# Kernel optimization log

Measured on AMD Instinct MI355X. Metric: run time of the kernel, lower is better.

The kernel has to match this reference:

```python
import jax, jax.numpy as jnp
import numpy as np

NBOXES = 4096
MAX_BS = 128
NDIM = 3
NPAIRS = 8192
INV4PI = 0.07957747154594767  # 1/(4*pi), 3D Laplace kernel constant


def setup_inputs() -> dict:
    key = jax.random.key(0)
    k1, k2, k3, k4 = jax.random.split(key, 4)
    q_vec = jax.random.normal(k1, (NBOXES, MAX_BS), dtype=jnp.float32)
    XX_list = jax.random.uniform(k2, (NBOXES, MAX_BS, NDIM), dtype=jnp.float32)
    bs_list = jax.random.randint(k3, (NBOXES,), 0, MAX_BS, dtype=jnp.int32)
    uq_boxes = jax.random.randint(k4, (NPAIRS, 2), 0, NBOXES, dtype=jnp.int32)
    return {"q_vec": q_vec, "XX_list": XX_list, "bs_list": bs_list, "uq_boxes": uq_boxes}


def reference(q_vec, XX_list, bs_list, uq_boxes):
    # Batched gather-kernel-matvec-scatter translation (addto_translation with
    # self_bool=False, kappa=0 => 3D Laplace kernel 1/(4*pi*r)).
    nboxes, max_bs = q_vec.shape
    u_boxes = uq_boxes[:, 0]
    q_boxes = uq_boxes[:, 1]

    Xu = XX_list[u_boxes]  # [P, B, 3] gather target points
    Xq = XX_list[q_boxes]  # [P, B, 3] gather source points

    # pairwise squared distances without materializing [P,B,B,3] diffs
    nu = jnp.sum(Xu * Xu, axis=-1)  # [P, B]
    nq = jnp.sum(Xq * Xq, axis=-1)  # [P, B]
    r2 = nu[:, :, None] + nq[:, None, :] - 2.0 * jnp.einsum('pid,pjd->pij', Xu, Xq)
    r2 = jnp.maximum(r2, 0.0)
    nz = r2 > 0.0
    K = jnp.where(nz, INV4PI / jnp.sqrt(jnp.where(nz, r2, 1.0)), 0.0)  # [P, B, B]

    cols = jnp.arange(max_bs, dtype=jnp.int32)
    col_mask = (cols[None, :] < bs_list[q_boxes][:, None]).astype(q_vec.dtype)  # valid src pts
    row_mask = (cols[None, :] < bs_list[u_boxes][:, None]).astype(q_vec.dtype)  # valid trg pts

    qv = q_vec[q_boxes] * col_mask                         # gather + zero_col_bnd
    out = jnp.einsum('pij,pj->pi', K, qv) * row_mask       # batched kernel matvec

    u_vec = jnp.zeros_like(q_vec).at[u_boxes].add(out)     # index_add_ scatter
    return u_vec
```

## Files before the change

### kernel.cpp

```cpp
#include <hip/hip_runtime.h>

#define NBOXES 4096
#define MAX_BS 128
#define INV4PI 0.07957747154594767f

template<int NR>
__device__ __forceinline__ void sweep(const float4* __restrict__ sq, int bs_q,
                                      const float* xu, const float* yu,
                                      const float* zu, float* acc)
{
    int j = 0;
    for (; j + 8 <= bs_q; j += 8) {
        float4 s[8];
#pragma unroll
        for (int c = 0; c < 8; ++c) s[c] = sq[j + c];
#pragma unroll
        for (int c = 0; c < 8; ++c) {
#pragma unroll
            for (int r = 0; r < NR; ++r) {
                const float dx = xu[r] - s[c].x;
                const float dy = yu[r] - s[c].y;
                const float dz = zu[r] - s[c].z;
                const float r2 = dx * dx + dy * dy + dz * dz;
                float rinv = __builtin_amdgcn_rsqf(r2);
                rinv = (r2 > 0.0f) ? rinv : 0.0f;
                acc[r] = fmaf(s[c].w, rinv, acc[r]);
            }
        }
    }
    for (; j < bs_q; ++j) {
        const float4 s = sq[j];
#pragma unroll
        for (int r = 0; r < NR; ++r) {
            const float dx = xu[r] - s.x;
            const float dy = yu[r] - s.y;
            const float dz = zu[r] - s.z;
            const float r2 = dx * dx + dy * dy + dz * dz;
            float rinv = __builtin_amdgcn_rsqf(r2);
            rinv = (r2 > 0.0f) ? rinv : 0.0f;
            acc[r] = fmaf(s.w, rinv, acc[r]);
        }
    }
}

__global__ __launch_bounds__(128) void fmm_pair2_kernel(
    const float* __restrict__ q_vec,
    const float* __restrict__ XX,
    const int*   __restrict__ bs_list,
    const int2*  __restrict__ uq_boxes,
    int npairs,
    float*       __restrict__ out)
{
    const int w = threadIdx.x >> 6;
    const int t = threadIdx.x & 63;
    const int p = blockIdx.x * 2 + w;

    __shared__ float4 sq[2][MAX_BS];

    const int2 uq = uq_boxes[p];
    const int u = uq.x;
    const int q = uq.y;
    const int bs_u = bs_list[u];
    const int bs_q = bs_list[q];

    {
        const float* Xq = XX + (size_t)q * (MAX_BS * 3);
        const float* qv = q_vec + (size_t)q * MAX_BS;
#pragma unroll
        for (int r = 0; r < 2; ++r) {
            const int jj = t + 64 * r;
            const float x = Xq[3 * jj + 0];
            const float y = Xq[3 * jj + 1];
            const float z = Xq[3 * jj + 2];
            const float wt = (jj < bs_q) ? qv[jj] * INV4PI : 0.0f;
            sq[w][jj] = make_float4(x, y, z, wt);
        }
    }

    const float* Xu = XX + (size_t)u * (MAX_BS * 3);
    float xu[2], yu[2], zu[2];
#pragma unroll
    for (int r = 0; r < 2; ++r) {
        const int ii = t + 64 * r;
        xu[r] = Xu[3 * ii + 0];
        yu[r] = Xu[3 * ii + 1];
        zu[r] = Xu[3 * ii + 2];
    }

    __syncthreads();

    float acc[2] = {0.0f, 0.0f};
    if (bs_u > 64) {
        sweep<2>(sq[w], bs_q, xu, yu, zu, acc);
    } else if (bs_u > 0) {
        sweep<1>(sq[w], bs_q, xu, yu, zu, acc);
    }

    float* orow = out + (size_t)u * MAX_BS;
    if (t < bs_u)      atomicAdd(orow + t,      acc[0]);
    if (t + 64 < bs_u) atomicAdd(orow + t + 64, acc[1]);
}

extern "C" void kernel_launch(void* const* d_in, const int* in_sizes, int n_in,
                              void* d_out, int out_size, void* d_ws, size_t ws_size,
                              hipStream_t stream) {
    const float* q_vec    = (const float*)d_in[0];
    const float* XX_list  = (const float*)d_in[1];
    const int*   bs_list  = (const int*)d_in[2];
    const int2*  uq_boxes = (const int2*)d_in[3];
    float* out = (float*)d_out;

    const int npairs = in_sizes[3] / 2;

    hipMemsetAsync(d_out, 0, (size_t)out_size * sizeof(float), stream);

    fmm_pair2_kernel<<<npairs / 2, 128, 0, stream>>>(
        q_vec, XX_list, bs_list, uq_boxes, npairs, out);
}
```

Baseline: 93.16 us.

## Precompute packed points with half-norms and expand distance via dot products

A prep kernel packs every point as float4 holding xyz and half its squared norm into workspace. The pair kernel then computes r2/2 as h_u + h_q - x_u·x_q with three FMAs and drops the r2>0 check for pairs of distinct boxes. The 1/sqrt2 and 1/(4π) factors move into one final scale. Pairs from the same box keep the direct difference form. Source data is read straight from global memory, so shared-memory staging and the block barrier are gone. Pairs with an empty box exit early, and each block now holds 4 waves. The expanded form risks cancellation error, or a negative argument to the rsqrt, when points are close together. It also adds an extra launch and about 8 MB of workspace traffic.

```diff
diff --git a/kernel.cpp b/kernel.cpp
--- a/kernel.cpp
+++ b/kernel.cpp
@@ -2,103 +2,119 @@
 
 #define NBOXES 4096
 #define MAX_BS 128
+#define NPTS (NBOXES * MAX_BS)
 #define INV4PI 0.07957747154594767f
+#define RSQRT2 0.70710678118654752f
+
+__global__ __launch_bounds__(256) void prep_kernel(
+    const float* __restrict__ XX, float4* __restrict__ pk)
+{
+    const int i = blockIdx.x * 256 + threadIdx.x;
+    const float x = XX[3 * i + 0];
+    const float y = XX[3 * i + 1];
+    const float z = XX[3 * i + 2];
+    const float h = 0.5f * fmaf(x, x, fmaf(y, y, z * z));
+    pk[i] = make_float4(x, y, z, h);
+}
 
 template<int NR>
-__device__ __forceinline__ void sweep(const float4* __restrict__ sq, int bs_q,
-                                      const float* xu, const float* yu,
-                                      const float* zu, float* acc)
+__device__ __forceinline__ void sweep_exp(
+    const float4* __restrict__ pq, const float* __restrict__ qv, int bs_q,
+    const float4* A, float* acc)
 {
     int j = 0;
     for (; j + 8 <= bs_q; j += 8) {
-        float4 s[8];
+        float4 s[8]; float wq[8];
 #pragma unroll
-        for (int c = 0; c < 8; ++c) s[c] = sq[j + c];
+        for (int c = 0; c < 8; ++c) { s[c] = pq[j + c]; wq[c] = qv[j + c]; }
 #pragma unroll
         for (int c = 0; c < 8; ++c) {
 #pragma unroll
             for (int r = 0; r < NR; ++r) {
-                const float dx = xu[r] - s[c].x;
-                const float dy = yu[r] - s[c].y;
-                const float dz = zu[r] - s[c].z;
-                const float r2 = dx * dx + dy * dy + dz * dz;
-                float rinv = __builtin_amdgcn_rsqf(r2);
-                rinv = (r2 > 0.0f) ? rinv : 0.0f;
-                acc[r] = fmaf(s[c].w, rinv, acc[r]);
+                float g = fmaf(-A[r].x, s[c].x, A[r].w);
+                g = fmaf(-A[r].y, s[c].y, g);
+                g = fmaf(-A[r].z, s[c].z, g);
+                g += s[c].w;
+                acc[r] = fmaf(wq[c], __builtin_amdgcn_rsqf(g), acc[r]);
             }
         }
     }
     for (; j < bs_q; ++j) {
-        const float4 s = sq[j];
+        const float4 s = pq[j]; const float wq = qv[j];
 #pragma unroll
         for (int r = 0; r < NR; ++r) {
-            const float dx = xu[r] - s.x;
-            const float dy = yu[r] - s.y;
-            const float dz = zu[r] - s.z;
-            const float r2 = dx * dx + dy * dy + dz * dz;
-            float rinv = __builtin_amdgcn_rsqf(r2);
-            rinv = (r2 > 0.0f) ? rinv : 0.0f;
-            acc[r] = fmaf(s.w, rinv, acc[r]);
+            float g = fmaf(-A[r].x, s.x, A[r].w);
+            g = fmaf(-A[r].y, s.y, g);
+            g = fmaf(-A[r].z, s.z, g);
+            g += s.w;
+            acc[r] = fmaf(wq, __builtin_amdgcn_rsqf(g), acc[r]);
         }
     }
 }
 
-__global__ __launch_bounds__(128) void fmm_pair2_kernel(
-    const float* __restrict__ q_vec,
-    const float* __restrict__ XX,
-    const int*   __restrict__ bs_list,
-    const int2*  __restrict__ uq_boxes,
+template<int NR>
+__device__ __forceinline__ void sweep_self(
+    const float4* __restrict__ pq, const float* __restrict__ qv, int bs_q,
+    const float4* A, float* acc)
+{
+    for (int j = 0; j < bs_q; ++j) {
+        const float4 s = pq[j]; const float wq = qv[j];
+#pragma unroll
+        for (int r = 0; r < NR; ++r) {
+            const float dx = A[r].x - s.x;
+            const float dy = A[r].y - s.y;
+            const float dz = A[r].z - s.z;
+            const float r2 = fmaf(dx, dx, fmaf(dy, dy, dz * dz));
+            float rv = __builtin_amdgcn_rsqf(r2);
+            rv = (r2 > 0.0f) ? rv : 0.0f;
+            acc[r] = fmaf(wq, rv, acc[r]);
+        }
+    }
+}
+
+__global__ __launch_bounds__(256) void fmm_kernel(
+    const float*  __restrict__ q_vec,
+    const float4* __restrict__ pk,
+    const int*    __restrict__ bs_list,
+    const int2*   __restrict__ uq_boxes,
     int npairs,
-    float*       __restrict__ out)
+    float*        __restrict__ out)
 {
     const int w = threadIdx.x >> 6;
     const int t = threadIdx.x & 63;
-    const int p = blockIdx.x * 2 + w;
-
-    __shared__ float4 sq[2][MAX_BS];
+    const int p = blockIdx.x * 4 + w;
+    if (p >= npairs) return;
 
     const int2 uq = uq_boxes[p];
-    const int u = uq.x;
-    const int q = uq.y;
+    const int u = __builtin_amdgcn_readfirstlane(uq.x);
+    const int q = __builtin_amdgcn_readfirstlane(uq.y);
     const int bs_u = bs_list[u];
     const int bs_q = bs_list[q];
+    if (bs_u == 0 || bs_q == 0) return;
 
-    {
-        const float* Xq = XX + (size_t)q * (MAX_BS * 3);
-        const float* qv = q_vec + (size_t)q * MAX_BS;
-#pragma unroll
-        for (int r = 0; r < 2; ++r) {
-            const int jj = t + 64 * r;
-            const float x = Xq[3 * jj + 0];
-            const float y = Xq[3 * jj + 1];
-            const float z = Xq[3 * jj + 2];
-            const float wt = (jj < bs_q) ? qv[jj] * INV4PI : 0.0f;
-            sq[w][jj] = make_float4(x, y, z, wt);
-        }
-    }
+    const float4* __restrict__ pq = pk + (size_t)q * MAX_BS;
+    const float*  __restrict__ qv = q_vec + (size_t)q * MAX_BS;
 
-    const float* Xu = XX + (size_t)u * (MAX_BS * 3);
-    float xu[2], yu[2], zu[2];
-#pragma unroll
-    for (int r = 0; r < 2; ++r) {
-        const int ii = t + 64 * r;
-        xu[r] = Xu[3 * ii + 0];
-        yu[r] = Xu[3 * ii + 1];
-        zu[r] = Xu[3 * ii + 2];
-    }
-
-    __syncthreads();
+    float4 A[2];
+    A[0] = pk[(size_t)u * MAX_BS + t];
+    const bool two = (bs_u > 64);
+    if (two) A[1] = pk[(size_t)u * MAX_BS + t + 64];
 
     float acc[2] = {0.0f, 0.0f};
-    if (bs_u > 64) {
-        sweep<2>(sq[w], bs_q, xu, yu, zu, acc);
-    } else if (bs_u > 0) {
-        sweep<1>(sq[w], bs_q, xu, yu, zu, acc);
+    float scale;
+    if (u != q) {
+        if (two) sweep_exp<2>(pq, qv, bs_q, A, acc);
+        else     sweep_exp<1>(pq, qv, bs_q, A, acc);
+        scale = INV4PI * RSQRT2;
+    } else {
+        if (two) sweep_self<2>(pq, qv, bs_q, A, acc);
+        else     sweep_self<1>(pq, qv, bs_q, A, acc);
+        scale = INV4PI;
     }
 
     float* orow = out + (size_t)u * MAX_BS;
-    if (t < bs_u)      atomicAdd(orow + t,      acc[0]);
-    if (t + 64 < bs_u) atomicAdd(orow + t + 64, acc[1]);
+    if (t < bs_u)               atomicAdd(orow + t,      acc[0] * scale);
+    if (two && t + 64 < bs_u)   atomicAdd(orow + t + 64, acc[1] * scale);
 }
 
 extern "C" void kernel_launch(void* const* d_in, const int* in_sizes, int n_in,
@@ -112,8 +128,12 @@
 
     const int npairs = in_sizes[3] / 2;
 
+    float4* pk = (float4*)d_ws;
+
     hipMemsetAsync(d_out, 0, (size_t)out_size * sizeof(float), stream);
 
-    fmm_pair2_kernel<<<npairs / 2, 128, 0, stream>>>(
-        q_vec, XX_list, bs_list, uq_boxes, npairs, out);
+    prep_kernel<<<NPTS / 256, 256, 0, stream>>>(XX_list, pk);
+
+    fmm_kernel<<<(npairs + 3) / 4, 256, 0, stream>>>(
+        q_vec, pk, bs_list, uq_boxes, npairs, out);
 }
```

Measured after the change: 93.62 us. Within noise of the previous version (+0.5%).
